# Optimization experiments

Hardware: AMD Instinct MI355X
Metric: run time of the kernel (lower is better)

The kernel has to match this reference:

```python
import jax, jax.numpy as jnp
import numpy as np

B, L, E, H, EXP = 2, 2048, 1024, 16, 4
D = E // H
EPS = 1e-5

def layernorm(x, g, b):
    mu = jnp.mean(x, axis=-1, keepdims=True)
    var = jnp.var(x, axis=-1, keepdims=True)
    return (x - mu) * jax.lax.rsqrt(var + EPS) * g + b

def setup_inputs() -> dict:
    key = jax.random.key(0)
    ks = jax.random.split(key, 12)
    s = 0.02
    return {
        "x": jax.random.normal(ks[0], (B, L, E), dtype=jnp.float32),
        "ln1_g": jnp.ones((E,), jnp.float32),
        "ln1_b": jnp.zeros((E,), jnp.float32),
        "W_qkv": jax.random.normal(ks[1], (E, 3 * E), dtype=jnp.float32) * s,
        "W_proj": jax.random.normal(ks[2], (E, E), dtype=jnp.float32) * s,
        "b_proj": jnp.zeros((E,), jnp.float32),
        "ln2_g": jnp.ones((E,), jnp.float32),
        "ln2_b": jnp.zeros((E,), jnp.float32),
        "W1": jax.random.normal(ks[3], (E, EXP * E), dtype=jnp.float32) * s,
        "b1": jnp.zeros((EXP * E,), jnp.float32),
        "W2": jax.random.normal(ks[4], (EXP * E, E), dtype=jnp.float32) * s,
        "b2": jnp.zeros((E,), jnp.float32),
    }

def reference(x, ln1_g, ln1_b, W_qkv, W_proj, b_proj, ln2_g, ln2_b, W1, b1, W2, b2):
    # --- attention sub-block (pre-LN) ---
    h = layernorm(x, ln1_g, ln1_b)                      # [B,L,E]
    qkv = h @ W_qkv                                      # [B,L,3E]
    q, k, v = jnp.split(qkv, 3, axis=-1)
    q = q.reshape(B, L, H, D).transpose(0, 2, 1, 3)      # [B,H,L,D]
    k = k.reshape(B, L, H, D).transpose(0, 2, 1, 3)
    v = v.reshape(B, L, H, D).transpose(0, 2, 1, 3)
    scale = jnp.sqrt(jnp.float32(E))                     # NOTE: module divides by sqrt(E), not sqrt(D)
    att = jnp.einsum('bhqd,bhkd->bhqk', q, k) / scale
    att = jax.nn.softmax(att, axis=-1)
    out = jnp.einsum('bhqk,bhkd->bhqd', att, v)          # [B,H,L,D]
    out = out.transpose(0, 2, 1, 3).reshape(B, L, E)
    x = x + out @ W_proj + b_proj                         # residual
    # --- feed-forward sub-block (pre-LN) ---
    h = layernorm(x, ln2_g, ln2_b)
    h = jax.nn.gelu(h @ W1 + b1, approximate=False)       # torch GELU is exact erf
    x = x + h @ W2 + b2
    return x
```

## Files before the change

kernel.cpp:

```cpp
#include <hip/hip_runtime.h>
#include <cstdint>
#include <cstddef>


typedef __bf16 bht;
typedef __attribute__((ext_vector_type(8))) __bf16 bf16x8;
typedef __attribute__((ext_vector_type(4))) __bf16 bf16x4;
typedef __attribute__((ext_vector_type(4))) float f32x4;
typedef __attribute__((ext_vector_type(4))) short short4v;

#define B_ 2
#define L_ 2048
#define E_ 1024
#define H_ 16
#define D_ 64
#define ROWS_ (B_ * L_)

#define QSCALE_ 0.045084441f

__device__ __forceinline__ void glds16(const void* g, void* l) {
    __builtin_amdgcn_global_load_lds(
        (const __attribute__((address_space(1))) unsigned int*)g,
        (__attribute__((address_space(3))) unsigned int*)l, 16, 0, 0);
}

__device__ __forceinline__ short4v as_s4(bf16x4 v) {
    return __builtin_bit_cast(short4v, v);
}

__device__ __forceinline__ float fast_exp2(float x) {
#if __has_builtin(__builtin_amdgcn_exp2f)
    return __builtin_amdgcn_exp2f(x);
#else
    return exp2f(x);
#endif
}

__global__ __launch_bounds__(256)
void transpose_cast(const float* __restrict__ in, bht* __restrict__ out, int R, int C) {
    __shared__ float tile[32][33];
    const int bx = blockIdx.x * 32;
    const int by = blockIdx.y * 32;
    const int tx = threadIdx.x, ty = threadIdx.y;
    #pragma unroll
    for (int i = 0; i < 32; i += 8)
        tile[ty + i][tx] = in[(size_t)(by + ty + i) * C + bx + tx];
    __syncthreads();
    #pragma unroll
    for (int i = 0; i < 32; i += 8)
        out[(size_t)(bx + ty + i) * R + by + tx] = (bht)tile[tx][ty + i];
}

__global__ __launch_bounds__(256)
void ln_kernel(const float* __restrict__ x, const float* __restrict__ g,
               const float* __restrict__ b, bht* __restrict__ out) {
    const int row = blockIdx.x, t = threadIdx.x;
    const float4 v = ((const float4*)(x + (size_t)row * E_))[t];
    float s  = v.x + v.y + v.z + v.w;
    float ss = v.x*v.x + v.y*v.y + v.z*v.z + v.w*v.w;
    #pragma unroll
    for (int off = 32; off > 0; off >>= 1) {
        s  += __shfl_down(s, off);
        ss += __shfl_down(ss, off);
    }
    __shared__ float red[8];
    const int wave = t >> 6, lane = t & 63;
    if (lane == 0) { red[wave] = s; red[4 + wave] = ss; }
    __syncthreads();
    s  = red[0] + red[1] + red[2] + red[3];
    ss = red[4] + red[5] + red[6] + red[7];
    const float mean = s * (1.0f / (float)E_);
    const float var  = ss * (1.0f / (float)E_) - mean * mean;
    const float rstd = rsqrtf(var + 1e-5f);
    const float4 gv = ((const float4*)g)[t];
    const float4 bv = ((const float4*)b)[t];
    bf16x4 o;
    o.x = (bht)((v.x - mean) * rstd * gv.x + bv.x);
    o.y = (bht)((v.y - mean) * rstd * gv.y + bv.y);
    o.z = (bht)((v.z - mean) * rstd * gv.z + bv.z);
    o.w = (bht)((v.w - mean) * rstd * gv.w + bv.w);
    *(bf16x4*)(out + (size_t)row * E_ + t * 4) = o;
}

enum { EPI_QKV = 0, EPI_RESID = 1, EPI_GELU = 2 };

template <int EPI>
__global__ __launch_bounds__(512, 2)
void gemm256(const bht* __restrict__ A, const bht* __restrict__ Bt,
             const float* __restrict__ bias, void* __restrict__ outp,
             bht* __restrict__ qo, bht* __restrict__ ko, bht* __restrict__ vto,
             int M, int N, int K) {
    __shared__ __align__(16) char smem_[98304];
    const int t = threadIdx.x;
    const int lane = t & 63, wave = t >> 6;
    const int lane15 = lane & 15, quad = lane >> 4;
    const int waveM = wave >> 2, waveN = wave & 3;
    const int bm = blockIdx.y * 256, bn = blockIdx.x * 256;

    f32x4 acc[8][4];
    #pragma unroll
    for (int i = 0; i < 8; ++i)
        #pragma unroll
        for (int j = 0; j < 4; ++j)
            acc[i][j] = f32x4{0.f, 0.f, 0.f, 0.f};

    const int apc = ((quad ^ ((lane15 >> 1) & 3)) & 3) * 8;
    const int aoff = waveM * 4096 + lane15 * 32 + apc;
    const int boff = waveN * 2048 + lane15 * 32 + apc;

    auto stage_step = [&](int s, int op, int bufi) {
        const int k0 = s * 32;
        const bht* src = op ? Bt : A;
        const int rb = op ? bn : bm;
        char* dst = smem_ + (size_t)bufi * 32768 + op * 16384;
        #pragma unroll
        for (int i = 0; i < 2; ++i) {
            const int g = i * 512 + t;
            const int row = g >> 2;
            const int c = ((g & 3) ^ ((row >> 1) & 3)) * 8;
            glds16(src + (size_t)(rb + row) * K + k0 + c, dst + (size_t)g * 16);
        }
    };

    const int NT = K >> 5;
    stage_step(0, 0, 0); stage_step(0, 1, 0);
    stage_step(1, 0, 1); stage_step(1, 1, 1);

    int cb = 0;
    for (int s = 0; s < NT; ++s) {
        const int nb2 = (cb >= 1) ? cb - 1 : 2;
        if (s + 2 < NT) {
            stage_step(s + 2, 0, nb2);
            asm volatile("s_waitcnt vmcnt(6)" ::: "memory");
        } else if (s + 1 < NT) {
            asm volatile("s_waitcnt vmcnt(4)" ::: "memory");
        } else {
            asm volatile("s_waitcnt vmcnt(0)" ::: "memory");
        }
        __builtin_amdgcn_s_barrier();
        asm volatile("" ::: "memory");

        const bht* Au = (const bht*)(smem_ + (size_t)cb * 32768);
        const bht* Bu = (const bht*)(smem_ + (size_t)cb * 32768 + 16384);
        bf16x8 af[8], bfv[4];
        #pragma unroll
        for (int m = 0; m < 8; ++m)
            af[m] = *(const bf16x8*)(Au + aoff + m * 512);
        #pragma unroll
        for (int n = 0; n < 4; ++n)
            bfv[n] = *(const bf16x8*)(Bu + boff + n * 512);
        if (s + 2 < NT) stage_step(s + 2, 1, nb2);
        asm volatile("s_waitcnt lgkmcnt(0)" ::: "memory");
        __builtin_amdgcn_s_setprio(1);
        #pragma unroll
        for (int m = 0; m < 8; ++m)
            #pragma unroll
            for (int n = 0; n < 4; ++n)
                acc[m][n] = __builtin_amdgcn_mfma_f32_16x16x32_bf16(af[m], bfv[n], acc[m][n], 0, 0, 0);
        __builtin_amdgcn_s_setprio(0);
        __builtin_amdgcn_s_barrier();
        asm volatile("" ::: "memory");

        cb = (cb == 2) ? 0 : cb + 1;
    }

    if constexpr (EPI == EPI_GELU) {
        #pragma unroll
        for (int m = 0; m < 8; ++m) {
            const int row0 = bm + waveM * 128 + m * 16 + quad * 4;
            #pragma unroll
            for (int n = 0; n < 4; ++n) {
                const int col = bn + waveN * 64 + n * 16 + lane15;
                #pragma unroll
                for (int r = 0; r < 4; ++r) {
                    float v = acc[m][n][r] + bias[col];
                    v = 0.5f * v * (1.0f + erff(v * 0.70710678118654752f));
                    ((bht*)outp)[(size_t)(row0 + r) * N + col] = (bht)v;
                }
            }
        }
    } else {
        const int b = bm >> 11, l0 = bm & 2047;
        if (bn >= 2048) {
            bht* Vtile = (bht*)smem_;
            #pragma unroll
            for (int h = 0; h < 2; ++h) {
                if ((waveN >> 1) == h) {
                    #pragma unroll
                    for (int m = 0; m < 8; ++m) {
                        const int rl0 = waveM * 128 + m * 16 + quad * 4;
                        #pragma unroll
                        for (int n = 0; n < 4; ++n) {
                            const int c = (waveN & 1) * 64 + n * 16 + lane15;
                            #pragma unroll
                            for (int r = 0; r < 4; ++r)
                                Vtile[(size_t)c * 264 + rl0 + r] = (bht)acc[m][n][r];
                        }
                    }
                }
                __syncthreads();
                #pragma unroll
                for (int it = 0; it < 4; ++it) {
                    const int c2 = it * 32 + (t >> 4);
                    const int cg = (bn - 2048) + h * 128 + c2;
                    const int hh = cg >> 6, d = cg & 63;
                    const int bh2 = b * H_ + hh;
                    #pragma unroll
                    for (int half2 = 0; half2 < 2; ++half2) {
                        const int ch = (t & 15) + 16 * half2;
                        bf16x8 vv = *(const bf16x8*)(Vtile + (size_t)c2 * 264 + ch * 8);
                        if (d & 8)
                            vv = __builtin_shufflevector(vv, vv, 4, 5, 6, 7, 0, 1, 2, 3);
                        *(bf16x8*)(vto + ((size_t)bh2 * D_ + d) * L_ + l0 + ch * 8) = vv;
                    }
                }
                __syncthreads();
            }
        } else {
            #pragma unroll
            for (int m = 0; m < 8; ++m) {
                const int row0 = bm + waveM * 128 + m * 16 + quad * 4;
                #pragma unroll
                for (int n = 0; n < 4; ++n) {
                    const int col = bn + waveN * 64 + n * 16 + lane15;
                    const int seg = col >> 10;
                    const int c = col & 1023;
                    const int hh = c >> 6, d = c & 63;
                    #pragma unroll
                    for (int r = 0; r < 4; ++r) {
                        const int mrow = row0 + r;
                        const int bb = mrow >> 11, l = mrow & 2047;
                        const int bh2 = bb * H_ + hh;
                        const float v = acc[m][n][r];
                        if (seg == 0)
                            qo[((size_t)bh2 * L_ + l) * D_ + d] = (bht)(v * QSCALE_);
                        else
                            ko[((size_t)bh2 * L_ + l) * D_ + d] = (bht)v;
                    }
                }
            }
        }
    }
    (void)M;
}

template <int EPI>
__global__ __launch_bounds__(256)
void gemm_pipe64(const bht* __restrict__ A, const bht* __restrict__ Bt,
                 const float* __restrict__ bias, const float* __restrict__ resid,
                 void* __restrict__ outp, int M, int N, int K) {
    __shared__ __align__(16) char smem_[49152];
    const int t = threadIdx.x;
    const int lane = t & 63, wave = t >> 6;
    const int lane15 = lane & 15, quad = lane >> 4;
    const int waveM = wave >> 1, waveN = wave & 1;

    const int flat = blockIdx.y * gridDim.x + blockIdx.x;
    const int xcd = flat & 7;
    const int w = flat >> 3;
    const int bm = (xcd * (gridDim.y >> 3) + (w >> 3)) * 64;
    const int bn = (w & 7) * 128;

    f32x4 acc[2][4];
    #pragma unroll
    for (int i = 0; i < 2; ++i)
        #pragma unroll
        for (int j = 0; j < 4; ++j)
            acc[i][j] = f32x4{0.f, 0.f, 0.f, 0.f};

    const int swz = lane15 & 7;

    auto stage = [&](int s, int bufi) {
        const int k0 = s * 64;
        char* base = smem_ + (size_t)bufi * 24576;
        #pragma unroll
        for (int i = 0; i < 2; ++i) {
            const int g = i * 256 + t;
            const int row = g >> 3;
            const int col = ((g & 7) ^ (row & 7)) * 8;
            glds16(A + (size_t)(bm + row) * K + k0 + col, base + (size_t)g * 16);
        }
        #pragma unroll
        for (int i = 0; i < 4; ++i) {
            const int g = i * 256 + t;
            const int row = g >> 3;
            const int col = ((g & 7) ^ (row & 7)) * 8;
            glds16(Bt + (size_t)(bn + row) * K + k0 + col, base + 8192 + (size_t)g * 16);
        }
    };

    const int NT = K >> 6;
    stage(0, 0);
    for (int s = 0; s < NT; ++s) {
        if (s + 1 < NT) {
            stage(s + 1, (s + 1) & 1);
            asm volatile("s_waitcnt vmcnt(6)" ::: "memory");
        } else {
            asm volatile("s_waitcnt vmcnt(0)" ::: "memory");
        }
        __builtin_amdgcn_s_barrier();
        asm volatile("" ::: "memory");

        const bht* As = (const bht*)(smem_ + (size_t)(s & 1) * 24576);
        const bht* Bs = (const bht*)(smem_ + (size_t)(s & 1) * 24576 + 8192);
        __builtin_amdgcn_s_setprio(1);
        #pragma unroll
        for (int kk = 0; kk < 2; ++kk) {
            const int pc = ((kk * 4 + quad) ^ swz) * 8;
            bf16x8 af[2], bfv[4];
            #pragma unroll
            for (int i = 0; i < 2; ++i)
                af[i] = *(const bf16x8*)(As + (waveM * 32 + i * 16 + lane15) * 64 + pc);
            #pragma unroll
            for (int j = 0; j < 4; ++j)
                bfv[j] = *(const bf16x8*)(Bs + (waveN * 64 + j * 16 + lane15) * 64 + pc);
            #pragma unroll
            for (int i = 0; i < 2; ++i)
                #pragma unroll
                for (int j = 0; j < 4; ++j)
                    acc[i][j] = __builtin_amdgcn_mfma_f32_16x16x32_bf16(af[i], bfv[j], acc[i][j], 0, 0, 0);
        }
        __builtin_amdgcn_s_setprio(0);
        asm volatile("s_waitcnt lgkmcnt(0)" ::: "memory");
        __builtin_amdgcn_s_barrier();
        asm volatile("" ::: "memory");
    }

    #pragma unroll
    for (int i = 0; i < 2; ++i) {
        const int row0 = bm + waveM * 32 + i * 16 + quad * 4;
        #pragma unroll
        for (int j = 0; j < 4; ++j) {
            const int col = bn + waveN * 64 + j * 16 + lane15;
            #pragma unroll
            for (int r = 0; r < 4; ++r) {
                const int m = row0 + r;
                float v = acc[i][j][r];
                if (EPI == EPI_RESID) {
                    ((float*)outp)[(size_t)m * N + col] =
                        v + bias[col] + resid[(size_t)m * N + col];
                } else {
                    v += bias[col];
                    v = 0.5f * v * (1.0f + erff(v * 0.70710678118654752f));
                    ((bht*)outp)[(size_t)m * N + col] = (bht)v;
                }
            }
        }
    }
}

#define KT_ 128
#define NT_ (L_ / KT_)

__global__ __launch_bounds__(256)
void attn_kernel(const bht* __restrict__ Q, const bht* __restrict__ Kb,
                 const bht* __restrict__ Vt, bht* __restrict__ O) {
    __shared__ __align__(16) bht Ks[KT_ * 64];
    __shared__ __align__(16) bht Vs[64 * KT_];
    __shared__ float Ls[4][16];
    const int t = threadIdx.x;
    const int lane = t & 63, wave = t >> 6;
    const int lane15 = lane & 15, quad = lane >> 4;
    const int bh = blockIdx.x, qt = blockIdx.y;

    const bht* Qh = Q  + (size_t)bh * L_ * D_;
    const bht* Kh = Kb + (size_t)bh * L_ * D_;
    const bht* Vh = Vt + (size_t)bh * D_ * L_;

    const int q0 = qt * 64 + wave * 16;

    bf16x8 aq[2];
    #pragma unroll
    for (int kc = 0; kc < 2; ++kc)
        aq[kc] = *(const bf16x8*)(Qh + (size_t)(q0 + lane15) * D_ + kc * 32 + quad * 8);

    f32x4 o_acc[4];
    #pragma unroll
    for (int db = 0; db < 4; ++db) o_acc[db] = f32x4{0.f, 0.f, 0.f, 0.f};
    float l_sum = 0.f;

    const int pc0 = (quad ^ (lane15 & 7)) * 8;
    const int pc1 = pc0 ^ 32;
    const int vhalf4 = ((quad & 1) ^ ((lane15 >> 3) & 1)) * 4;

    auto stageK = [&](int kt2) {
        const int key0 = kt2 * KT_;
        #pragma unroll
        for (int i = 0; i < 4; ++i) {
            const int g = i * 256 + t;
            const int krow = g >> 3;
            const int ksc = ((g & 7) ^ (krow & 7)) * 8;
            glds16(Kh + (size_t)(key0 + krow) * D_ + ksc, (char*)Ks + (size_t)g * 16);
        }
    };
    auto stageV = [&](int kt2) {
        const int key0 = kt2 * KT_;
        #pragma unroll
        for (int i = 0; i < 4; ++i) {
            const int g = i * 256 + t;
            const int vrow = g >> 4;
            const int vsc = ((g & 15) ^ (vrow & 7)) * 8;
            glds16(Vh + (size_t)vrow * L_ + key0 + vsc, (char*)Vs + (size_t)g * 16);
        }
    };

    stageK(0);
    stageV(0);

    for (int kt = 0; kt < NT_; ++kt) {
        asm volatile("s_waitcnt vmcnt(4) lgkmcnt(0)" ::: "memory");
        __builtin_amdgcn_s_barrier();

        __builtin_amdgcn_s_setprio(1);
        short4v pk[8];
        #pragma unroll
        for (int nb = 0; nb < 8; ++nb) {
            const bf16x8 ak0 = *(const bf16x8*)(Ks + (nb * 16 + lane15) * 64 + pc0);
            const bf16x8 ak1 = *(const bf16x8*)(Ks + (nb * 16 + lane15) * 64 + pc1);
            f32x4 st = __builtin_amdgcn_mfma_f32_16x16x32_bf16(
                ak0, aq[0], f32x4{0.f, 0.f, 0.f, 0.f}, 0, 0, 0);
            st = __builtin_amdgcn_mfma_f32_16x16x32_bf16(ak1, aq[1], st, 0, 0, 0);
            bf16x4 pkv;
            #pragma unroll
            for (int r = 0; r < 4; ++r) {
                const float pv = fast_exp2(st[r]);
                l_sum += pv;
                pkv[r] = (bht)pv;
            }
            pk[nb] = as_s4(pkv);
        }
        __builtin_amdgcn_s_setprio(0);

        asm volatile("s_waitcnt vmcnt(0) lgkmcnt(0)" ::: "memory");
        __builtin_amdgcn_s_barrier();
        if (kt + 1 < NT_) stageK(kt + 1);

        __builtin_amdgcn_s_setprio(1);
        #pragma unroll
        for (int nb = 0; nb < 8; ++nb) {
            #pragma unroll
            for (int db = 0; db < 4; ++db) {
                const int row = db * 16 + lane15;
                const int c16 = (nb * 2 + (quad >> 1)) ^ (row & 7);
                const bf16x4 bv = *(const bf16x4*)(Vs + row * KT_ + c16 * 8 + vhalf4);
                o_acc[db] = __builtin_amdgcn_mfma_f32_16x16x16bf16_1k(
                    pk[nb], as_s4(bv), o_acc[db], 0, 0, 0);
            }
        }
        __builtin_amdgcn_s_setprio(0);

        asm volatile("s_waitcnt lgkmcnt(0)" ::: "memory");
        __builtin_amdgcn_s_barrier();
        if (kt + 1 < NT_) stageV(kt + 1);
    }

    l_sum += __shfl_xor(l_sum, 16);
    l_sum += __shfl_xor(l_sum, 32);
    Ls[wave][lane15] = l_sum;
    asm volatile("s_waitcnt lgkmcnt(0)" ::: "memory");

    const int b = bh >> 4, h = bh & 15;
    #pragma unroll
    for (int r = 0; r < 4; ++r) {
        const int l = q0 + quad * 4 + r;
        const float inv = 1.0f / Ls[wave][quad * 4 + r];
        #pragma unroll
        for (int db = 0; db < 4; ++db)
            O[((size_t)b * L_ + l) * E_ + h * 64 + db * 16 + lane15] =
                (bht)(o_acc[db][r] * inv);
    }
}

extern "C" void kernel_launch(void* const* d_in, const int* in_sizes, int n_in,
                              void* d_out, int out_size, void* d_ws, size_t ws_size,
                              hipStream_t stream) {
    const float* x      = (const float*)d_in[0];
    const float* ln1_g  = (const float*)d_in[1];
    const float* ln1_b  = (const float*)d_in[2];
    const float* W_qkv  = (const float*)d_in[3];
    const float* W_proj = (const float*)d_in[4];
    const float* b_proj = (const float*)d_in[5];
    const float* ln2_g  = (const float*)d_in[6];
    const float* ln2_b  = (const float*)d_in[7];
    const float* W1     = (const float*)d_in[8];
    const float* b1     = (const float*)d_in[9];
    const float* W2     = (const float*)d_in[10];
    const float* b2     = (const float*)d_in[11];
    float* out = (float*)d_out;

    char* ws = (char*)d_ws;
    auto alloc = [&](size_t bytes) {
        char* p = ws;
        ws += (bytes + 255) & ~(size_t)255;
        return p;
    };
    bht*   WqkvT  = (bht*)alloc((size_t)3072 * 1024 * 2);
    bht*   WprojT = (bht*)alloc((size_t)1024 * 1024 * 2);
    bht*   W1T    = (bht*)alloc((size_t)4096 * 1024 * 2);
    bht*   W2T    = (bht*)alloc((size_t)1024 * 4096 * 2);
    bht*   hb     = (bht*)alloc((size_t)ROWS_ * E_ * 2);
    float* x1     = (float*)alloc((size_t)ROWS_ * E_ * 4);
    bht*   Qb     = (bht*)alloc((size_t)B_ * H_ * L_ * D_ * 2);
    bht*   Kbuf   = (bht*)alloc((size_t)B_ * H_ * L_ * D_ * 2);
    bht*   Vtb    = (bht*)alloc((size_t)B_ * H_ * D_ * L_ * 2);
    bht*   attno  = (bht*)alloc((size_t)ROWS_ * E_ * 2);
    bht*   ffn1   = Qb;

    transpose_cast<<<dim3(3072 / 32, 1024 / 32), dim3(32, 8), 0, stream>>>(W_qkv, WqkvT, 1024, 3072);
    transpose_cast<<<dim3(1024 / 32, 1024 / 32), dim3(32, 8), 0, stream>>>(W_proj, WprojT, 1024, 1024);
    transpose_cast<<<dim3(4096 / 32, 1024 / 32), dim3(32, 8), 0, stream>>>(W1, W1T, 1024, 4096);
    transpose_cast<<<dim3(1024 / 32, 4096 / 32), dim3(32, 8), 0, stream>>>(W2, W2T, 4096, 1024);

    ln_kernel<<<ROWS_, 256, 0, stream>>>(x, ln1_g, ln1_b, hb);

    gemm256<EPI_QKV><<<dim3(3072 / 256, ROWS_ / 256), 512, 0, stream>>>(
        hb, WqkvT, nullptr, nullptr, Qb, Kbuf, Vtb, ROWS_, 3072, 1024);

    attn_kernel<<<dim3(B_ * H_, L_ / 64), 256, 0, stream>>>(Qb, Kbuf, Vtb, attno);

    gemm_pipe64<EPI_RESID><<<dim3(1024 / 128, ROWS_ / 64), 256, 0, stream>>>(
        attno, WprojT, b_proj, x, x1, ROWS_, 1024, 1024);

    ln_kernel<<<ROWS_, 256, 0, stream>>>(x1, ln2_g, ln2_b, hb);

    gemm256<EPI_GELU><<<dim3(4096 / 256, ROWS_ / 256), 512, 0, stream>>>(
        hb, W1T, b1, ffn1, nullptr, nullptr, nullptr, ROWS_, 4096, 1024);

    gemm_pipe64<EPI_RESID><<<dim3(1024 / 128, ROWS_ / 64), 256, 0, stream>>>(
        ffn1, W2T, b2, x1, out, ROWS_, 1024, 4096);

    (void)in_sizes; (void)n_in; (void)out_size; (void)ws_size;
}
```

Before: 328.8 us.

## Switch gemm256 to double buffering with higher occupancy and interleaved A-fragment loads

The big GEMM kernel goes from a 3-stage LDS ring (96KB) to 2-stage double buffering (66KB), and launch bounds are raised from 2 to 4 blocks per CU. A fragments are now loaded from LDS inside the MFMA loop, one at a time, to cut register pressure. The explicit lgkmcnt waits are removed from both GEMM kernels so the compiler can interleave LDS reads with MFMAs. The shallower prefetch depth and tighter register budget under 4 waves/SIMD may raise latency exposure or cause spills. 4 blocks of 66KB may also exceed the LDS capacity per CU, so the occupancy gain is uncertain.

```diff
diff --git a/kernel.cpp b/kernel.cpp
--- a/kernel.cpp
+++ b/kernel.cpp
@@ -85,12 +85,12 @@
 enum { EPI_QKV = 0, EPI_RESID = 1, EPI_GELU = 2 };
 
 template <int EPI>
-__global__ __launch_bounds__(512, 2)
+__global__ __launch_bounds__(512, 4)
 void gemm256(const bht* __restrict__ A, const bht* __restrict__ Bt,
              const float* __restrict__ bias, void* __restrict__ outp,
              bht* __restrict__ qo, bht* __restrict__ ko, bht* __restrict__ vto,
              int M, int N, int K) {
-    __shared__ __align__(16) char smem_[98304];
+    __shared__ __align__(16) char smem_[67584];
     const int t = threadIdx.x;
     const int lane = t & 63, wave = t >> 6;
     const int lane15 = lane & 15, quad = lane >> 4;
@@ -108,11 +108,11 @@
     const int aoff = waveM * 4096 + lane15 * 32 + apc;
     const int boff = waveN * 2048 + lane15 * 32 + apc;
 
-    auto stage_step = [&](int s, int op, int bufi) {
+    auto stage_step = [&](int s, int op) {
         const int k0 = s * 32;
         const bht* src = op ? Bt : A;
         const int rb = op ? bn : bm;
-        char* dst = smem_ + (size_t)bufi * 32768 + op * 16384;
+        char* dst = smem_ + (size_t)(s & 1) * 32768 + op * 16384;
         #pragma unroll
         for (int i = 0; i < 2; ++i) {
             const int g = i * 512 + t;
@@ -123,45 +123,36 @@
     };
 
     const int NT = K >> 5;
-    stage_step(0, 0, 0); stage_step(0, 1, 0);
-    stage_step(1, 0, 1); stage_step(1, 1, 1);
-
-    int cb = 0;
+    stage_step(0, 0); stage_step(0, 1);
+
     for (int s = 0; s < NT; ++s) {
-        const int nb2 = (cb >= 1) ? cb - 1 : 2;
-        if (s + 2 < NT) {
-            stage_step(s + 2, 0, nb2);
-            asm volatile("s_waitcnt vmcnt(6)" ::: "memory");
-        } else if (s + 1 < NT) {
-            asm volatile("s_waitcnt vmcnt(4)" ::: "memory");
+        if (s + 1 < NT) {
+            stage_step(s + 1, 0);
+            asm volatile("s_waitcnt vmcnt(2)" ::: "memory");
         } else {
             asm volatile("s_waitcnt vmcnt(0)" ::: "memory");
         }
         __builtin_amdgcn_s_barrier();
         asm volatile("" ::: "memory");
 
-        const bht* Au = (const bht*)(smem_ + (size_t)cb * 32768);
-        const bht* Bu = (const bht*)(smem_ + (size_t)cb * 32768 + 16384);
-        bf16x8 af[8], bfv[4];
-        #pragma unroll
-        for (int m = 0; m < 8; ++m)
-            af[m] = *(const bf16x8*)(Au + aoff + m * 512);
+        const bht* Au = (const bht*)(smem_ + (size_t)(s & 1) * 32768);
+        const bht* Bu = (const bht*)(smem_ + (size_t)(s & 1) * 32768 + 16384);
+        bf16x8 bfv[4];
         #pragma unroll
         for (int n = 0; n < 4; ++n)
             bfv[n] = *(const bf16x8*)(Bu + boff + n * 512);
-        if (s + 2 < NT) stage_step(s + 2, 1, nb2);
-        asm volatile("s_waitcnt lgkmcnt(0)" ::: "memory");
+        if (s + 1 < NT) stage_step(s + 1, 1);
         __builtin_amdgcn_s_setprio(1);
         #pragma unroll
-        for (int m = 0; m < 8; ++m)
+        for (int m = 0; m < 8; ++m) {
+            const bf16x8 afm = *(const bf16x8*)(Au + aoff + m * 512);
             #pragma unroll
             for (int n = 0; n < 4; ++n)
-                acc[m][n] = __builtin_amdgcn_mfma_f32_16x16x32_bf16(af[m], bfv[n], acc[m][n], 0, 0, 0);
+                acc[m][n] = __builtin_amdgcn_mfma_f32_16x16x32_bf16(afm, bfv[n], acc[m][n], 0, 0, 0);
+        }
         __builtin_amdgcn_s_setprio(0);
         __builtin_amdgcn_s_barrier();
         asm volatile("" ::: "memory");
-
-        cb = (cb == 2) ? 0 : cb + 1;
     }
 
     if constexpr (EPI == EPI_GELU) {
@@ -307,21 +298,19 @@
         #pragma unroll
         for (int kk = 0; kk < 2; ++kk) {
             const int pc = ((kk * 4 + quad) ^ swz) * 8;
-            bf16x8 af[2], bfv[4];
-            #pragma unroll
-            for (int i = 0; i < 2; ++i)
-                af[i] = *(const bf16x8*)(As + (waveM * 32 + i * 16 + lane15) * 64 + pc);
+            bf16x8 bfv[4];
             #pragma unroll
             for (int j = 0; j < 4; ++j)
                 bfv[j] = *(const bf16x8*)(Bs + (waveN * 64 + j * 16 + lane15) * 64 + pc);
             #pragma unroll
-            for (int i = 0; i < 2; ++i)
+            for (int i = 0; i < 2; ++i) {
+                const bf16x8 afi = *(const bf16x8*)(As + (waveM * 32 + i * 16 + lane15) * 64 + pc);
                 #pragma unroll
                 for (int j = 0; j < 4; ++j)
-                    acc[i][j] = __builtin_amdgcn_mfma_f32_16x16x32_bf16(af[i], bfv[j], acc[i][j], 0, 0, 0);
+                    acc[i][j] = __builtin_amdgcn_mfma_f32_16x16x32_bf16(afi, bfv[j], acc[i][j], 0, 0, 0);
+            }
         }
         __builtin_amdgcn_s_setprio(0);
-        asm volatile("s_waitcnt lgkmcnt(0)" ::: "memory");
         __builtin_amdgcn_s_barrier();
         asm volatile("" ::: "memory");
     }
```

Measured after the change: 653.1 us. 98.6% more time.
